# Kernel optimization log

Hardware: AMD Instinct MI355X
Metric: run time of the kernel (lower is better)

## Reference

```python
import jax, jax.numpy as jnp
import numpy as np

GROUP = 32  # quantization group size along the last (contraction-adjacent) axis


def dequant(vals, scales):
    # vals: [R, N] int values in [-127,127]; scales: [R, N//GROUP] fp32
    r, n = vals.shape
    w = vals.reshape(r, n // GROUP, GROUP).astype(jnp.float32) * scales[:, :, None]
    return w.reshape(r, n)


def setup_inputs() -> dict:
    key = jax.random.key(0)
    k1, k2, k3, k4, k5 = jax.random.split(key, 5)
    T, D, R = 16384, 4096, 64  # tokens, d_model, lora rank
    x = jax.random.normal(k1, (T, D), dtype=jnp.float32)
    qa_vals = jax.random.randint(k2, (R, D), -127, 128, dtype=jnp.int32)
    qa_scales = jax.random.uniform(k3, (R, D // GROUP), dtype=jnp.float32) * 0.02
    qb_vals = jax.random.randint(k4, (D, R), -127, 128, dtype=jnp.int32)
    qb_scales = jax.random.uniform(k5, (D, R // GROUP), dtype=jnp.float32) * 0.02
    return {"x": x, "qa_vals": qa_vals, "qa_scales": qa_scales,
            "qb_vals": qb_vals, "qb_scales": qb_scales}


def reference(x, qa_vals, qa_scales, qb_vals, qb_scales):
    # Dequantize LoRA weights, then two chained F.linear matmuls.
    a = dequant(qa_vals, qa_scales)   # [rank, in_features]
    b = dequant(qb_vals, qb_scales)   # [out_features, rank]
    h = x @ a.T                        # [T, rank]
    return h @ b.T                     # [T, out_features]
```

## Files before the change

kernel.cpp:

```cpp
#include <hip/hip_runtime.h>
#include <hip/hip_bf16.h>
#include <stdint.h>
#include <stddef.h>

#define D_MODEL 4096
#define RANK    64
#define KC      512
#define NCH     (D_MODEL / KC)
#define M_BLK   32

typedef __attribute__((ext_vector_type(4)))  float f32x4;
typedef __attribute__((ext_vector_type(16))) float f32x16;
typedef __attribute__((ext_vector_type(8)))  short bf16x8;

__device__ inline short f2bf1(float f) {
    union { __hip_bfloat16 t; short s; } c;
    c.t = __float2bfloat16(f);
    return c.s;
}
__device__ inline uint32_t pkbf(float a, float b) {
    union { __hip_bfloat162 t; uint32_t u; } c;
    c.t = __float22bfloat162_rn(make_float2(a, b));
    return c.u;
}

__global__ __launch_bounds__(256) void dequant_pack_kernel(
        const int* __restrict__ qa, const float* __restrict__ qas,
        const int* __restrict__ qb, const float* __restrict__ qbs,
        short* __restrict__ apk, short* __restrict__ bpk) {
    const int idx = blockIdx.x * 256 + threadIdx.x;
    const int l = idx & 63, t = idx >> 6;
    {
        const int n = t & 3, kb = t >> 2;
        const int r = 16 * n + (l & 15);
        const int kbase = kb * 32 + ((l >> 4) << 3);
        const int* q = qa + (size_t)r * D_MODEL + kbase;
        const float s = qas[r * (D_MODEL / 32) + kb];
        bf16x8 o;
        #pragma unroll
        for (int j = 0; j < 8; ++j) o[j] = f2bf1((float)q[j] * s);
        *(bf16x8*)(apk + (size_t)idx * 8) = o;
    }
    {
        const int ks = t & 3, cb = t >> 2;
        const int d = cb * 32 + (l & 31);
        const int rbase = ks * 16 + ((l >> 5) << 3);
        const int* q = qb + (size_t)d * RANK + rbase;
        const float s = qbs[d * 2 + (ks >> 1)];
        bf16x8 o;
        #pragma unroll
        for (int j = 0; j < 8; ++j) o[j] = f2bf1((float)q[j] * s);
        *(bf16x8*)(bpk + (size_t)idx * 8) = o;
    }
}

__global__ __launch_bounds__(512, 4) void fused_kernel(
        const float* __restrict__ x, const short* __restrict__ apk,
        const short* __restrict__ bpk, float* __restrict__ out) {
    __shared__ __align__(16) char smem[65536 + 5120];
    float* red   = (float*)smem;
    short* h_lds = (short*)(smem + 65536);

    const int tid  = threadIdx.x;
    const int lane = tid & 63;
    const int wave = tid >> 6;
    const int rb   = blockIdx.x * M_BLK;

    const int srow = tid >> 7;
    const int scol = (tid & 127) << 2;
    const float* xb = x + (size_t)rb * D_MODEL;

    f32x4 xr[8];
    #pragma unroll
    for (int r = 0; r < 8; ++r)
        xr[r] = *(const f32x4*)(xb + (size_t)(r * 4 + srow) * D_MODEL + scol);
    #pragma unroll
    for (int r = 0; r < 8; ++r) {
        const int row = r * 4 + srow;
        int byte = row * 1024 + (scol << 1);
        byte ^= (row & 7) << 4;
        union { uint32_t w[2]; uint2 u; } p;
        p.w[0] = pkbf(xr[r][0], xr[r][1]);
        p.w[1] = pkbf(xr[r][2], xr[r][3]);
        *(uint2*)(smem + byte) = p.u;
    }
    #pragma unroll
    for (int r = 0; r < 8; ++r)
        xr[r] = *(const f32x4*)(xb + (size_t)(r * 4 + srow) * D_MODEL + KC + scol);
    __syncthreads();

    f32x4 acc[2][4];
    #pragma unroll
    for (int m = 0; m < 2; ++m)
        #pragma unroll
        for (int n = 0; n < 4; ++n)
            acc[m][n] = (f32x4){0.f, 0.f, 0.f, 0.f};

    for (int c = 0; c < NCH; ++c) {
        const char* sb = smem + (c & 1) * 32768;
        #pragma unroll
        for (int ks = 0; ks < 2; ++ks) {
            const int kin = wave * 64 + ks * 32 + ((lane >> 4) << 3);
            bf16x8 af[2];
            #pragma unroll
            for (int m = 0; m < 2; ++m) {
                const int row = m * 16 + (lane & 15);
                int byte = row * 1024 + (kin << 1);
                byte ^= (row & 7) << 4;
                af[m] = *(const bf16x8*)(sb + byte);
            }
            const int kbg = c * 16 + wave * 2 + ks;
            #pragma unroll
            for (int n = 0; n < 4; ++n) {
                bf16x8 bf = *(const bf16x8*)(apk + ((size_t)((kbg * 4 + n) * 64 + lane) << 3));
                #pragma unroll
                for (int m = 0; m < 2; ++m)
                    acc[m][n] = __builtin_amdgcn_mfma_f32_16x16x32_bf16(
                        af[m], bf, acc[m][n], 0, 0, 0);
            }
        }
        if (c < NCH - 1) {
            char* sw = smem + ((c + 1) & 1) * 32768;
            #pragma unroll
            for (int r = 0; r < 8; ++r) {
                const int row = r * 4 + srow;
                int byte = row * 1024 + (scol << 1);
                byte ^= (row & 7) << 4;
                union { uint32_t w[2]; uint2 u; } p;
                p.w[0] = pkbf(xr[r][0], xr[r][1]);
                p.w[1] = pkbf(xr[r][2], xr[r][3]);
                *(uint2*)(sw + byte) = p.u;
            }
            if (c < NCH - 2) {
                #pragma unroll
                for (int r = 0; r < 8; ++r)
                    xr[r] = *(const f32x4*)(xb + (size_t)(r * 4 + srow) * D_MODEL
                                            + (size_t)(c + 2) * KC + scol);
            }
        }
        __syncthreads();
    }

    const int r4 = (lane >> 4) << 2;
    if (wave < 4) {
        #pragma unroll
        for (int m = 0; m < 2; ++m)
            #pragma unroll
            for (int n = 0; n < 4; ++n)
                #pragma unroll
                for (int j = 0; j < 4; ++j)
                    red[(wave * 32 + m * 16 + r4 + j) * 68 + n * 16 + (lane & 15)] =
                        acc[m][n][j];
    }
    __syncthreads();
    if (wave >= 4) {
        #pragma unroll
        for (int m = 0; m < 2; ++m)
            #pragma unroll
            for (int n = 0; n < 4; ++n)
                #pragma unroll
                for (int j = 0; j < 4; ++j)
                    red[((wave - 4) * 32 + m * 16 + r4 + j) * 68 + n * 16 + (lane & 15)] +=
                        acc[m][n][j];
    }
    __syncthreads();
    for (int e = tid; e < 32 * 64; e += 512) {
        const int r = e >> 6, cc = e & 63;
        float s = red[(0 * 32 + r) * 68 + cc] + red[(1 * 32 + r) * 68 + cc]
                + red[(2 * 32 + r) * 68 + cc] + red[(3 * 32 + r) * 68 + cc];
        h_lds[r * 80 + cc] = f2bf1(s);
    }
    __syncthreads();

    bf16x8 hf[4];
    #pragma unroll
    for (int ks = 0; ks < 4; ++ks)
        hf[ks] = *(const bf16x8*)(h_lds + (lane & 31) * 80 + ks * 16 + ((lane >> 5) << 3));

    #pragma unroll
    for (int n = 0; n < 16; ++n) {
        const int cb32 = wave * 16 + n;
        const int col  = cb32 * 32 + (lane & 31);
        f32x16 a2;
        #pragma unroll
        for (int j = 0; j < 16; ++j) a2[j] = 0.f;
        #pragma unroll
        for (int ks = 0; ks < 4; ++ks) {
            bf16x8 bf = *(const bf16x8*)(bpk + ((size_t)((cb32 * 4 + ks) * 64 + lane) << 3));
            a2 = __builtin_amdgcn_mfma_f32_32x32x16_bf16(hf[ks], bf, a2, 0, 0, 0);
        }
        #pragma unroll
        for (int reg = 0; reg < 16; ++reg) {
            const int r = (reg & 3) + 8 * (reg >> 2) + ((lane >> 5) << 2);
            out[(size_t)(rb + r) * D_MODEL + col] = a2[reg];
        }
    }
}

extern "C" void kernel_launch(void* const* d_in, const int* in_sizes, int n_in,
                              void* d_out, int out_size, void* d_ws, size_t ws_size,
                              hipStream_t stream) {
    (void)n_in; (void)out_size; (void)ws_size;
    const float* x   = (const float*)d_in[0];
    const int*   qa  = (const int*)d_in[1];
    const float* qas = (const float*)d_in[2];
    const int*   qb  = (const int*)d_in[3];
    const float* qbs = (const float*)d_in[4];
    float* out = (float*)d_out;

    const int T = in_sizes[0] / D_MODEL;

    short* apk = (short*)d_ws;
    short* bpk = apk + (size_t)RANK * D_MODEL;

    dequant_pack_kernel<<<128, 256, 0, stream>>>(qa, qas, qb, qbs, apk, bpk);
    fused_kernel<<<T / M_BLK, 512, 0, stream>>>(x, apk, bpk, out);
}
```

Before: 144.4 us.

## Halve row tile to 16 with 256-thread blocks and 16x16 MFMA second GEMM

Shrinks the per-block token tile from 32 to 16 rows and the block from 8 to 4 waves, giving twice as many blocks and halving LDS use. The K split across waves becomes 4-way, which removes one reduction pass. The second GEMM moves from 32x32x16 to 16x16x32 MFMA, with the B weights repacked to match. The intent is better occupancy and load balance. In exchange, each block re-reads the A and B weight fragments for only half as many rows, which doubles weight traffic per output.

```diff
diff --git a/kernel.cpp b/kernel.cpp
--- a/kernel.cpp
+++ b/kernel.cpp
@@ -7,10 +7,9 @@
 #define RANK    64
 #define KC      512
 #define NCH     (D_MODEL / KC)
-#define M_BLK   32
+#define M_BLK   16
 
 typedef __attribute__((ext_vector_type(4)))  float f32x4;
-typedef __attribute__((ext_vector_type(16))) float f32x16;
 typedef __attribute__((ext_vector_type(8)))  short bf16x8;
 
 __device__ inline short f2bf1(float f) {
@@ -42,11 +41,11 @@
         *(bf16x8*)(apk + (size_t)idx * 8) = o;
     }
     {
-        const int ks = t & 3, cb = t >> 2;
-        const int d = cb * 32 + (l & 31);
-        const int rbase = ks * 16 + ((l >> 5) << 3);
+        const int ks = t & 1, cb = t >> 1;
+        const int d = cb * 16 + (l & 15);
+        const int rbase = ks * 32 + ((l >> 4) << 3);
         const int* q = qb + (size_t)d * RANK + rbase;
-        const float s = qbs[d * 2 + (ks >> 1)];
+        const float s = qbs[d * 2 + ks];
         bf16x8 o;
         #pragma unroll
         for (int j = 0; j < 8; ++j) o[j] = f2bf1((float)q[j] * s);
@@ -54,12 +53,12 @@
     }
 }
 
-__global__ __launch_bounds__(512, 4) void fused_kernel(
+__global__ __launch_bounds__(256, 4) void fused_kernel(
         const float* __restrict__ x, const short* __restrict__ apk,
         const short* __restrict__ bpk, float* __restrict__ out) {
-    __shared__ __align__(16) char smem[65536 + 5120];
+    __shared__ __align__(16) char smem[32768 + 2560];
     float* red   = (float*)smem;
-    short* h_lds = (short*)(smem + 65536);
+    short* h_lds = (short*)(smem + 32768);
 
     const int tid  = threadIdx.x;
     const int lane = tid & 63;
@@ -73,10 +72,10 @@
     f32x4 xr[8];
     #pragma unroll
     for (int r = 0; r < 8; ++r)
-        xr[r] = *(const f32x4*)(xb + (size_t)(r * 4 + srow) * D_MODEL + scol);
+        xr[r] = *(const f32x4*)(xb + (size_t)(r * 2 + srow) * D_MODEL + scol);
     #pragma unroll
     for (int r = 0; r < 8; ++r) {
-        const int row = r * 4 + srow;
+        const int row = r * 2 + srow;
         int byte = row * 1024 + (scol << 1);
         byte ^= (row & 7) << 4;
         union { uint32_t w[2]; uint2 u; } p;
@@ -86,44 +85,34 @@
     }
     #pragma unroll
     for (int r = 0; r < 8; ++r)
-        xr[r] = *(const f32x4*)(xb + (size_t)(r * 4 + srow) * D_MODEL + KC + scol);
+        xr[r] = *(const f32x4*)(xb + (size_t)(r * 2 + srow) * D_MODEL + KC + scol);
     __syncthreads();
 
-    f32x4 acc[2][4];
+    f32x4 acc[4];
     #pragma unroll
-    for (int m = 0; m < 2; ++m)
-        #pragma unroll
-        for (int n = 0; n < 4; ++n)
-            acc[m][n] = (f32x4){0.f, 0.f, 0.f, 0.f};
+    for (int n = 0; n < 4; ++n) acc[n] = (f32x4){0.f, 0.f, 0.f, 0.f};
 
     for (int c = 0; c < NCH; ++c) {
-        const char* sb = smem + (c & 1) * 32768;
+        const char* sb = smem + (c & 1) * 16384;
         #pragma unroll
-        for (int ks = 0; ks < 2; ++ks) {
-            const int kin = wave * 64 + ks * 32 + ((lane >> 4) << 3);
-            bf16x8 af[2];
-            #pragma unroll
-            for (int m = 0; m < 2; ++m) {
-                const int row = m * 16 + (lane & 15);
-                int byte = row * 1024 + (kin << 1);
-                byte ^= (row & 7) << 4;
-                af[m] = *(const bf16x8*)(sb + byte);
-            }
-            const int kbg = c * 16 + wave * 2 + ks;
+        for (int s = 0; s < 4; ++s) {
+            const int kin = wave * 128 + s * 32 + ((lane >> 4) << 3);
+            const int row = lane & 15;
+            int byte = row * 1024 + (kin << 1);
+            byte ^= (row & 7) << 4;
+            bf16x8 af = *(const bf16x8*)(sb + byte);
+            const int kbg = c * 16 + wave * 4 + s;
             #pragma unroll
             for (int n = 0; n < 4; ++n) {
                 bf16x8 bf = *(const bf16x8*)(apk + ((size_t)((kbg * 4 + n) * 64 + lane) << 3));
-                #pragma unroll
-                for (int m = 0; m < 2; ++m)
-                    acc[m][n] = __builtin_amdgcn_mfma_f32_16x16x32_bf16(
-                        af[m], bf, acc[m][n], 0, 0, 0);
+                acc[n] = __builtin_amdgcn_mfma_f32_16x16x32_bf16(af, bf, acc[n], 0, 0, 0);
             }
         }
         if (c < NCH - 1) {
-            char* sw = smem + ((c + 1) & 1) * 32768;
+            char* sw = smem + ((c + 1) & 1) * 16384;
             #pragma unroll
             for (int r = 0; r < 8; ++r) {
-                const int row = r * 4 + srow;
+                const int row = r * 2 + srow;
                 int byte = row * 1024 + (scol << 1);
                 byte ^= (row & 7) << 4;
                 union { uint32_t w[2]; uint2 u; } p;
@@ -134,7 +123,7 @@
             if (c < NCH - 2) {
                 #pragma unroll
                 for (int r = 0; r < 8; ++r)
-                    xr[r] = *(const f32x4*)(xb + (size_t)(r * 4 + srow) * D_MODEL
+                    xr[r] = *(const f32x4*)(xb + (size_t)(r * 2 + srow) * D_MODEL
                                             + (size_t)(c + 2) * KC + scol);
             }
         }
@@ -142,58 +131,38 @@
     }
 
     const int r4 = (lane >> 4) << 2;
-    if (wave < 4) {
+    #pragma unroll
+    for (int n = 0; n < 4; ++n)
         #pragma unroll
-        for (int m = 0; m < 2; ++m)
-            #pragma unroll
-            for (int n = 0; n < 4; ++n)
-                #pragma unroll
-                for (int j = 0; j < 4; ++j)
-                    red[(wave * 32 + m * 16 + r4 + j) * 68 + n * 16 + (lane & 15)] =
-                        acc[m][n][j];
-    }
+        for (int j = 0; j < 4; ++j)
+            red[(wave * 16 + r4 + j) * 68 + n * 16 + (lane & 15)] = acc[n][j];
     __syncthreads();
-    if (wave >= 4) {
-        #pragma unroll
-        for (int m = 0; m < 2; ++m)
-            #pragma unroll
-            for (int n = 0; n < 4; ++n)
-                #pragma unroll
-                for (int j = 0; j < 4; ++j)
-                    red[((wave - 4) * 32 + m * 16 + r4 + j) * 68 + n * 16 + (lane & 15)] +=
-                        acc[m][n][j];
-    }
-    __syncthreads();
-    for (int e = tid; e < 32 * 64; e += 512) {
+    for (int e = tid; e < 16 * 64; e += 256) {
         const int r = e >> 6, cc = e & 63;
-        float s = red[(0 * 32 + r) * 68 + cc] + red[(1 * 32 + r) * 68 + cc]
-                + red[(2 * 32 + r) * 68 + cc] + red[(3 * 32 + r) * 68 + cc];
+        float s = red[(0 * 16 + r) * 68 + cc] + red[(1 * 16 + r) * 68 + cc]
+                + red[(2 * 16 + r) * 68 + cc] + red[(3 * 16 + r) * 68 + cc];
         h_lds[r * 80 + cc] = f2bf1(s);
     }
     __syncthreads();
 
-    bf16x8 hf[4];
+    bf16x8 hf[2];
     #pragma unroll
-    for (int ks = 0; ks < 4; ++ks)
-        hf[ks] = *(const bf16x8*)(h_lds + (lane & 31) * 80 + ks * 16 + ((lane >> 5) << 3));
+    for (int ks = 0; ks < 2; ++ks)
+        hf[ks] = *(const bf16x8*)(h_lds + (lane & 15) * 80 + ks * 32 + ((lane >> 4) << 3));
 
-    #pragma unroll
-    for (int n = 0; n < 16; ++n) {
-        const int cb32 = wave * 16 + n;
-        const int col  = cb32 * 32 + (lane & 31);
-        f32x16 a2;
+    #pragma unroll 4
+    for (int n = 0; n < 64; ++n) {
+        const int cb = wave * 64 + n;
+        f32x4 a2 = (f32x4){0.f, 0.f, 0.f, 0.f};
         #pragma unroll
-        for (int j = 0; j < 16; ++j) a2[j] = 0.f;
+        for (int ks = 0; ks < 2; ++ks) {
+            bf16x8 bf = *(const bf16x8*)(bpk + ((size_t)((cb * 2 + ks) * 64 + lane) << 3));
+            a2 = __builtin_amdgcn_mfma_f32_16x16x32_bf16(hf[ks], bf, a2, 0, 0, 0);
+        }
+        const int col = cb * 16 + (lane & 15);
         #pragma unroll
-        for (int ks = 0; ks < 4; ++ks) {
-            bf16x8 bf = *(const bf16x8*)(bpk + ((size_t)((cb32 * 4 + ks) * 64 + lane) << 3));
-            a2 = __builtin_amdgcn_mfma_f32_32x32x16_bf16(hf[ks], bf, a2, 0, 0, 0);
-        }
-        #pragma unroll
-        for (int reg = 0; reg < 16; ++reg) {
-            const int r = (reg & 3) + 8 * (reg >> 2) + ((lane >> 5) << 2);
-            out[(size_t)(rb + r) * D_MODEL + col] = a2[reg];
-        }
+        for (int j = 0; j < 4; ++j)
+            out[(size_t)(rb + r4 + j) * D_MODEL + col] = a2[j];
     }
 }
 
@@ -214,5 +183,5 @@
     short* bpk = apk + (size_t)RANK * D_MODEL;
 
     dequant_pack_kernel<<<128, 256, 0, stream>>>(qa, qas, qb, qbs, apk, bpk);
-    fused_kernel<<<T / M_BLK, 512, 0, stream>>>(x, apk, bpk, out);
+    fused_kernel<<<T / M_BLK, 256, 0, stream>>>(x, apk, bpk, out);
 }
```

After: 155.2 us. 7.5% more time.
